# Optimization experiments

Measured on AMD Instinct MI355X. Metric: run time of the kernel, lower is better.

The kernel has to match this reference:

```python
import jax, jax.numpy as jnp
import numpy as np

N_EMBD = 2048
N_HEAD = 32
N_KV_HEADS = 8
HEAD_DIM = 64
N_REP = N_HEAD // N_KV_HEADS
MAX_SEQ_LEN = 4096
ROPE_THETA = 10000.0


def _precompute_freqs_cis(dim, end, theta=ROPE_THETA):
    freqs = 1.0 / theta ** (jnp.arange(0, dim, 2)[: dim // 2].astype(jnp.float32) / dim)
    t = jnp.arange(end, dtype=jnp.float32)
    freqs = jnp.outer(t, freqs)  # (end, dim//2)
    return jnp.cos(freqs), jnp.sin(freqs)


def setup_inputs() -> dict:
    key = jax.random.key(0)
    ks = jax.random.split(key, 5)
    B, S = 2, 2048
    x = jax.random.normal(ks[0], (B, S, N_EMBD), dtype=jnp.float32)
    # torch Linear(in, out, bias=False): y = x @ W.T, W is (out, in). We store (in, out).
    sc = 1.0 / np.sqrt(N_EMBD)
    wq = jax.random.normal(ks[1], (N_EMBD, N_EMBD), dtype=jnp.float32) * sc
    wk = jax.random.normal(ks[2], (N_EMBD, N_KV_HEADS * HEAD_DIM), dtype=jnp.float32) * sc
    wv = jax.random.normal(ks[3], (N_EMBD, N_KV_HEADS * HEAD_DIM), dtype=jnp.float32) * sc
    wo = jax.random.normal(ks[4], (N_EMBD, N_EMBD), dtype=jnp.float32) * sc
    freqs_cos, freqs_sin = _precompute_freqs_cis(HEAD_DIM, MAX_SEQ_LEN)
    return {"x": x, "wq": wq, "wk": wk, "wv": wv, "wo": wo,
            "freqs_cos": freqs_cos, "freqs_sin": freqs_sin}


def _apply_rotary(t, cos, sin):
    # t: (B, S, H, HD); interleaved real/imag pairs along last dim.
    shp = t.shape
    t2 = t.reshape(*shp[:-1], HEAD_DIM // 2, 2)
    r, i = t2[..., 0], t2[..., 1]
    out_r = r * cos - i * sin
    out_i = r * sin + i * cos
    return jnp.stack([out_r, out_i], axis=-1).reshape(shp)


def reference(x, wq, wk, wv, wo, freqs_cos, freqs_sin):
    B, S, _ = x.shape
    xq = (x @ wq).reshape(B, S, N_HEAD, HEAD_DIM)
    xk = (x @ wk).reshape(B, S, N_KV_HEADS, HEAD_DIM)
    xv = (x @ wv).reshape(B, S, N_KV_HEADS, HEAD_DIM)

    cos = freqs_cos[:S][None, :, None, :]  # (1, S, 1, HD/2)
    sin = freqs_sin[:S][None, :, None, :]
    xq = _apply_rotary(xq, cos, sin)
    xk = _apply_rotary(xk, cos, sin)

    # GQA: repeat KV heads (repeat_interleave along head dim)
    keys = jnp.repeat(xk, N_REP, axis=2)    # (B, S, H, HD)
    values = jnp.repeat(xv, N_REP, axis=2)

    scores = jnp.einsum('bqhd,bkhd->bhqk', xq, keys) / np.sqrt(HEAD_DIM)
    causal = jnp.tril(jnp.ones((S, S), dtype=bool))
    scores = jnp.where(causal, scores, -jnp.inf)
    probs = jax.nn.softmax(scores.astype(jnp.float32), axis=-1).astype(xq.dtype)
    out = jnp.einsum('bhqk,bkhd->bqhd', probs, values)  # (B, S, H, HD)
    out = out.reshape(B, S, N_EMBD)
    return out @ wo
```

## Files before the change

kernel.cpp:

```cpp
#include <hip/hip_runtime.h>
#include <hip/hip_fp16.h>
#include <stdint.h>

typedef _Float16 f16x8 __attribute__((ext_vector_type(8)));
typedef _Float16 f16x2 __attribute__((ext_vector_type(2)));
typedef float f32x4 __attribute__((ext_vector_type(4)));

#define B_ 2
#define S_ 2048
#define NE 2048
#define NH 32
#define NKV 8
#define HD 64
#define NTOK (B_ * S_)
#define QKVN 3072

__device__ __forceinline__ void gld_lds16(void* lds, const void* g) {
  __builtin_amdgcn_global_load_lds(
      (const __attribute__((address_space(1))) void*)g,
      (__attribute__((address_space(3))) void*)lds, 16, 0, 0);
}

__global__ void conv_x_kernel(const float* __restrict__ x,
                              _Float16* __restrict__ xo, int n2) {
  int i = blockIdx.x * 256 + threadIdx.x;
  if (i < n2) {
    float2 v = ((const float2*)x)[i];
    f16x2 h;
    h.x = (_Float16)v.x;
    h.y = (_Float16)v.y;
    ((f16x2*)xo)[i] = h;
  }
}

__global__ void tconv_kernel(const float* __restrict__ src,
                             _Float16* __restrict__ dst,
                             int srcN, int rowoff, int ldd) {
  __shared__ float tile[32][33];
  int n0 = blockIdx.x * 32, k0 = blockIdx.y * 32;
  int tx = threadIdx.x, ty = threadIdx.y;
  for (int i = ty; i < 32; i += 8)
    tile[i][tx] = src[(size_t)(k0 + i) * srcN + n0 + tx];
  __syncthreads();
  for (int i = ty; i < 32; i += 8)
    dst[(size_t)(rowoff + n0 + i) * ldd + k0 + tx] = (_Float16)tile[tx][i];
}

template <int OUT_F32>
__global__ __launch_bounds__(256, 2) void gemm_bt(
    const _Float16* __restrict__ A, const _Float16* __restrict__ Bt,
    void* __restrict__ Cout, int M, int N, int K) {
  __shared__ _Float16 As[128 * 32];
  __shared__ _Float16 Bs[128 * 32];
  const int tid = threadIdx.x;
  const int wave = tid >> 6, lane = tid & 63;
  const int qd = lane >> 4, ln = lane & 15;
  const int m0 = blockIdx.y * 128, n0 = blockIdx.x * 128;
  const int wm = (wave >> 1) * 64, wn = (wave & 1) * 64;

  f32x4 acc[4][4] = {};

  const int srow = (lane >> 2);
  const int scol = (lane & 3) * 8;

  for (int k0 = 0; k0 < K; k0 += 32) {
    __syncthreads();
#pragma unroll
    for (int it = 0; it < 2; ++it) {
      int r = wave * 32 + it * 16 + srow;
      gld_lds16(&As[(wave * 32 + it * 16) * 32],
                A + (size_t)(m0 + r) * K + k0 + scol);
      gld_lds16(&Bs[(wave * 32 + it * 16) * 32],
                Bt + (size_t)(n0 + r) * K + k0 + scol);
    }
    __syncthreads();
    f16x8 a[4], b[4];
#pragma unroll
    for (int mt = 0; mt < 4; ++mt)
      a[mt] = *(const f16x8*)&As[(wm + mt * 16 + ln) * 32 + qd * 8];
#pragma unroll
    for (int nt = 0; nt < 4; ++nt)
      b[nt] = *(const f16x8*)&Bs[(wn + nt * 16 + ln) * 32 + qd * 8];
#pragma unroll
    for (int mt = 0; mt < 4; ++mt)
#pragma unroll
      for (int nt = 0; nt < 4; ++nt)
        acc[mt][nt] =
            __builtin_amdgcn_mfma_f32_16x16x32_f16(a[mt], b[nt], acc[mt][nt], 0, 0, 0);
  }

#pragma unroll
  for (int mt = 0; mt < 4; ++mt) {
    int row = m0 + wm + mt * 16 + qd * 4;
#pragma unroll
    for (int nt = 0; nt < 4; ++nt) {
      int col = n0 + wn + nt * 16 + ln;
#pragma unroll
      for (int r = 0; r < 4; ++r) {
        if (OUT_F32)
          ((float*)Cout)[(size_t)(row + r) * N + col] = acc[mt][nt][r];
        else
          ((_Float16*)Cout)[(size_t)(row + r) * N + col] =
              (_Float16)acc[mt][nt][r];
      }
    }
  }
}

__global__ void rope_scatter_kernel(const _Float16* __restrict__ qkv,
                                    const float* __restrict__ fcos,
                                    const float* __restrict__ fsin,
                                    _Float16* __restrict__ Qb,
                                    _Float16* __restrict__ Kb) {
  const float QSC = 0.125f * 1.44269504088896f;
  int idx = blockIdx.x * 256 + threadIdx.x;
  int t = idx / 1280;
  int col = (idx - t * 1280) * 2;
  int b = t >> 11, s = t & 2047;
  float v0 = (float)qkv[(size_t)t * QKVN + col];
  float v1 = (float)qkv[(size_t)t * QKVN + col + 1];
  _Float16* dst;
  size_t off;
  int d;
  float sc;
  if (col < 2048) {
    int h = col >> 6;
    d = col & 63;
    dst = Qb;
    off = ((size_t)(b * NH + h) * S_ + s) * HD + d;
    sc = QSC;
  } else {
    int cc = col - 2048;
    int h = cc >> 6;
    d = cc & 63;
    dst = Kb;
    off = ((size_t)(b * NKV + h) * S_ + s) * HD + d;
    sc = 1.0f;
  }
  float c = fcos[s * 32 + (d >> 1)], sn = fsin[s * 32 + (d >> 1)];
  f16x2 o;
  o.x = (_Float16)((v0 * c - v1 * sn) * sc);
  o.y = (_Float16)((v0 * sn + v1 * c) * sc);
  *(f16x2*)(dst + off) = o;
}

__global__ void vtrans_kernel(const _Float16* __restrict__ qkv,
                              _Float16* __restrict__ Vtg) {
  __shared__ _Float16 tile[64][65];
  int t0 = blockIdx.x * 64;
  int kv = blockIdx.y, b = blockIdx.z;
  int tid = threadIdx.x;
  for (int slot = tid; slot < 4096; slot += 256) {
    int r = slot >> 6, c = slot & 63;
    tile[r][c] = qkv[(size_t)(b * S_ + t0 + r) * QKVN + 2560 + kv * 64 + c];
  }
  __syncthreads();
  size_t base = ((size_t)(b * NKV + kv) * HD) * S_;
  for (int slot = tid; slot < 4096; slot += 256) {
    int d = slot >> 6, r = slot & 63;
    Vtg[base + (size_t)d * S_ + t0 + r] = tile[r][d];
  }
}

__global__ __launch_bounds__(256, 2) void attn_kernel(
    const _Float16* __restrict__ Qb, const _Float16* __restrict__ Kb,
    const _Float16* __restrict__ Vtg, _Float16* __restrict__ Ob) {
  constexpr int LDK = 72;
  constexpr float M_SHIFT = 10.0f;
  __shared__ _Float16 Ks[64 * LDK];
  __shared__ _Float16 Vs[64 * LDK];
  __shared__ _Float16 Ps[4 * 32 * LDK];
  const int tid = threadIdx.x;
  const int wave = tid >> 6, lane = tid & 63;
  const int qd = lane >> 4, ln = lane & 15;
  const int h = blockIdx.y, b = blockIdx.z;
  const int kvh = h >> 2;

  const _Float16* Qh = Qb + ((size_t)(b * NH + h) * S_) * HD;
  const _Float16* Kh = Kb + ((size_t)(b * NKV + kvh) * S_) * HD;
  const _Float16* Vh = Vtg + ((size_t)(b * NKV + kvh) * HD) * S_;

  const int sr = tid >> 3;
  const int sc = (tid & 7) * 8;
  _Float16* Pw = &Ps[wave * 32 * LDK];

#pragma unroll
  for (int pass = 0; pass < 2; ++pass) {
    const int qt = pass ? blockIdx.x : (15 - blockIdx.x);
    const int q0 = qt * 128;
    const int nkt = 2 * qt + 2;

    f16x8 aq[2][2];
#pragma unroll
    for (int mt = 0; mt < 2; ++mt) {
      int qrow = q0 + mt * 64 + wave * 16 + ln;
      aq[mt][0] = *(const f16x8*)(Qh + (size_t)qrow * HD + qd * 8);
      aq[mt][1] = *(const f16x8*)(Qh + (size_t)qrow * HD + 32 + qd * 8);
    }

    f32x4 accO[2][4] = {};
    float lsum[2][4] = {};

    f16x8 kp[2], vp[2];
#pragma unroll
    for (int i = 0; i < 2; ++i) {
      kp[i] = *(const f16x8*)(Kh + (size_t)(i * 32 + sr) * HD + sc);
      vp[i] = *(const f16x8*)(Vh + (size_t)(i * 32 + sr) * S_ + sc);
    }
#pragma unroll
    for (int i = 0; i < 2; ++i) {
      *(f16x8*)&Ks[(i * 32 + sr) * LDK + sc] = kp[i];
      *(f16x8*)&Vs[(i * 32 + sr) * LDK + sc] = vp[i];
    }

    for (int kt = 0; kt < nkt; ++kt) {
      __syncthreads();
      if (kt + 1 < nkt) {
#pragma unroll
        for (int i = 0; i < 2; ++i) {
          kp[i] = *(const f16x8*)(Kh +
                                  (size_t)((kt + 1) * 64 + i * 32 + sr) * HD + sc);
          vp[i] = *(const f16x8*)(Vh + (size_t)(i * 32 + sr) * S_ +
                                  (kt + 1) * 64 + sc);
        }
      }

      f32x4 s[2][4];
#pragma unroll
      for (int mt = 0; mt < 2; ++mt)
#pragma unroll
        for (int nt = 0; nt < 4; ++nt)
          s[mt][nt] = (f32x4){-M_SHIFT, -M_SHIFT, -M_SHIFT, -M_SHIFT};
#pragma unroll
      for (int nt = 0; nt < 4; ++nt) {
        f16x8 b0 = *(const f16x8*)&Ks[(nt * 16 + ln) * LDK + qd * 8];
        f16x8 b1 = *(const f16x8*)&Ks[(nt * 16 + ln) * LDK + 32 + qd * 8];
#pragma unroll
        for (int mt = 0; mt < 2; ++mt) {
          s[mt][nt] = __builtin_amdgcn_mfma_f32_16x16x32_f16(aq[mt][0], b0,
                                                             s[mt][nt], 0, 0, 0);
          s[mt][nt] = __builtin_amdgcn_mfma_f32_16x16x32_f16(aq[mt][1], b1,
                                                             s[mt][nt], 0, 0, 0);
        }
      }

      const bool edge = (kt >= nkt - 2);
#pragma unroll
      for (int mt = 0; mt < 2; ++mt)
#pragma unroll
        for (int nt = 0; nt < 4; ++nt)
#pragma unroll
          for (int r = 0; r < 4; ++r) {
            float p = exp2f(s[mt][nt][r]);
            if (edge) {
              int key = kt * 64 + nt * 16 + ln;
              int qr = q0 + mt * 64 + wave * 16 + qd * 4 + r;
              if (key > qr) p = 0.f;
            }
            lsum[mt][r] += p;
            Pw[(mt * 16 + qd * 4 + r) * LDK + nt * 16 + ln] = (_Float16)p;
          }

      asm volatile("s_waitcnt lgkmcnt(0)" ::: "memory");
      f16x8 ap[2][2];
#pragma unroll
      for (int mt = 0; mt < 2; ++mt) {
        ap[mt][0] = *(const f16x8*)&Pw[(mt * 16 + ln) * LDK + qd * 8];
        ap[mt][1] = *(const f16x8*)&Pw[(mt * 16 + ln) * LDK + 32 + qd * 8];
      }
#pragma unroll
      for (int nt = 0; nt < 4; ++nt) {
        f16x8 bv0 = *(const f16x8*)&Vs[(nt * 16 + ln) * LDK + qd * 8];
        f16x8 bv1 = *(const f16x8*)&Vs[(nt * 16 + ln) * LDK + 32 + qd * 8];
#pragma unroll
        for (int mt = 0; mt < 2; ++mt) {
          accO[mt][nt] = __builtin_amdgcn_mfma_f32_16x16x32_f16(
              ap[mt][0], bv0, accO[mt][nt], 0, 0, 0);
          accO[mt][nt] = __builtin_amdgcn_mfma_f32_16x16x32_f16(
              ap[mt][1], bv1, accO[mt][nt], 0, 0, 0);
        }
      }

      __syncthreads();
      if (kt + 1 < nkt) {
#pragma unroll
        for (int i = 0; i < 2; ++i) {
          *(f16x8*)&Ks[(i * 32 + sr) * LDK + sc] = kp[i];
          *(f16x8*)&Vs[(i * 32 + sr) * LDK + sc] = vp[i];
        }
      }
    }

#pragma unroll
    for (int mt = 0; mt < 2; ++mt)
#pragma unroll
      for (int r = 0; r < 4; ++r) {
        float t = lsum[mt][r];
#pragma unroll
        for (int off = 1; off <= 8; off <<= 1) t += __shfl_xor(t, off);
        float inv = 1.f / t;
        int srow = q0 + mt * 64 + wave * 16 + qd * 4 + r;
        size_t base = ((size_t)(b * S_) + srow) * NE + h * HD;
#pragma unroll
        for (int nt = 0; nt < 4; ++nt)
          Ob[base + nt * 16 + ln] = (_Float16)(accO[mt][nt][r] * inv);
      }
  }
}

extern "C" void kernel_launch(void* const* d_in, const int* in_sizes, int n_in,
                              void* d_out, int out_size, void* d_ws,
                              size_t ws_size, hipStream_t stream) {
  const float* x = (const float*)d_in[0];
  const float* wq = (const float*)d_in[1];
  const float* wk = (const float*)d_in[2];
  const float* wv = (const float*)d_in[3];
  const float* wo = (const float*)d_in[4];
  const float* fcos = (const float*)d_in[5];
  const float* fsin = (const float*)d_in[6];

  char* ws = (char*)d_ws;
  _Float16* xb = (_Float16*)(ws);
  _Float16* wqkv_t = (_Float16*)(ws + 16777216);
  _Float16* wo_t = (_Float16*)(ws + 29360128);
  _Float16* qkv = (_Float16*)(ws + 37748736);
  _Float16* Qb = (_Float16*)(ws + 62914560);
  _Float16* Kb = (_Float16*)(ws + 79691776);
  _Float16* Vb = (_Float16*)(ws + 83886080);
  _Float16* Ob = (_Float16*)(ws + 88080384);

  conv_x_kernel<<<16384, 256, 0, stream>>>(x, xb, (NTOK * NE) / 2);

  dim3 tb(32, 8);
  tconv_kernel<<<dim3(64, 64), tb, 0, stream>>>(wq, wqkv_t, 2048, 0, 2048);
  tconv_kernel<<<dim3(16, 64), tb, 0, stream>>>(wk, wqkv_t, 512, 2048, 2048);
  tconv_kernel<<<dim3(16, 64), tb, 0, stream>>>(wv, wqkv_t, 512, 2560, 2048);
  tconv_kernel<<<dim3(64, 64), tb, 0, stream>>>(wo, wo_t, 2048, 0, 2048);

  gemm_bt<0><<<dim3(QKVN / 128, NTOK / 128), 256, 0, stream>>>(
      xb, wqkv_t, qkv, NTOK, QKVN, NE);

  rope_scatter_kernel<<<(NTOK * 1280) / 256, 256, 0, stream>>>(qkv, fcos, fsin,
                                                               Qb, Kb);
  vtrans_kernel<<<dim3(S_ / 64, NKV, B_), 256, 0, stream>>>(qkv, Vb);

  attn_kernel<<<dim3(8, NH, B_), 256, 0, stream>>>(Qb, Kb, Vb, Ob);

  gemm_bt<1><<<dim3(NE / 128, NTOK / 128), 256, 0, stream>>>(
      Ob, wo_t, d_out, NTOK, NE, NE);
}
```

Baseline: 349.9 us.

## Switch attention MFMAs to 32x32x16 tiles with XOR-swizzled K/V LDS layout

Rewrites the attention inner loops to use 32x32x16 f16 MFMA instructions instead of 16x16x32, so each wave owns 32 query rows and the fragment layout changes accordingly. K and V shared-memory tiles drop their row padding and use an XOR swizzle on 16-byte chunks to avoid bank conflicts. The intent is fewer MFMA issues and LDS reads per tile. In exchange the 16-element accumulators raise register pressure, and the row-sum reduction now needs one more shuffle step.

```diff
diff --git a/kernel.cpp b/kernel.cpp
--- a/kernel.cpp
+++ b/kernel.cpp
@@ -5,6 +5,7 @@
 typedef _Float16 f16x8 __attribute__((ext_vector_type(8)));
 typedef _Float16 f16x2 __attribute__((ext_vector_type(2)));
 typedef float f32x4 __attribute__((ext_vector_type(4)));
+typedef float f32x16 __attribute__((ext_vector_type(16)));
 
 #define B_ 2
 #define S_ 2048
@@ -165,14 +166,14 @@
 __global__ __launch_bounds__(256, 2) void attn_kernel(
     const _Float16* __restrict__ Qb, const _Float16* __restrict__ Kb,
     const _Float16* __restrict__ Vtg, _Float16* __restrict__ Ob) {
-  constexpr int LDK = 72;
+  constexpr int LDP = 72;
   constexpr float M_SHIFT = 10.0f;
-  __shared__ _Float16 Ks[64 * LDK];
-  __shared__ _Float16 Vs[64 * LDK];
-  __shared__ _Float16 Ps[4 * 32 * LDK];
+  __shared__ _Float16 Ks[64 * 64];
+  __shared__ _Float16 Vs[64 * 64];
+  __shared__ _Float16 Ps[4 * 32 * LDP];
   const int tid = threadIdx.x;
   const int wave = tid >> 6, lane = tid & 63;
-  const int qd = lane >> 4, ln = lane & 15;
+  const int mrow = lane & 31, half = lane >> 5;
   const int h = blockIdx.y, b = blockIdx.z;
   const int kvh = h >> 2;
 
@@ -181,8 +182,8 @@
   const _Float16* Vh = Vtg + ((size_t)(b * NKV + kvh) * HD) * S_;
 
   const int sr = tid >> 3;
-  const int sc = (tid & 7) * 8;
-  _Float16* Pw = &Ps[wave * 32 * LDK];
+  const int scc = tid & 7;
+  _Float16* Pw = &Ps[wave * 32 * LDP];
 
 #pragma unroll
   for (int pass = 0; pass < 2; ++pass) {
@@ -190,27 +191,26 @@
     const int q0 = qt * 128;
     const int nkt = 2 * qt + 2;
 
-    f16x8 aq[2][2];
-#pragma unroll
-    for (int mt = 0; mt < 2; ++mt) {
-      int qrow = q0 + mt * 64 + wave * 16 + ln;
-      aq[mt][0] = *(const f16x8*)(Qh + (size_t)qrow * HD + qd * 8);
-      aq[mt][1] = *(const f16x8*)(Qh + (size_t)qrow * HD + 32 + qd * 8);
-    }
-
-    f32x4 accO[2][4] = {};
-    float lsum[2][4] = {};
+    const int qrow = q0 + wave * 32 + mrow;
+    f16x8 aq[4];
+#pragma unroll
+    for (int kk = 0; kk < 4; ++kk)
+      aq[kk] = *(const f16x8*)(Qh + (size_t)qrow * HD + kk * 16 + half * 8);
+
+    f32x16 accO[2] = {};
+    float lsum[16] = {};
 
     f16x8 kp[2], vp[2];
 #pragma unroll
     for (int i = 0; i < 2; ++i) {
-      kp[i] = *(const f16x8*)(Kh + (size_t)(i * 32 + sr) * HD + sc);
-      vp[i] = *(const f16x8*)(Vh + (size_t)(i * 32 + sr) * S_ + sc);
+      kp[i] = *(const f16x8*)(Kh + (size_t)(i * 32 + sr) * HD + scc * 8);
+      vp[i] = *(const f16x8*)(Vh + (size_t)(i * 32 + sr) * S_ + scc * 8);
     }
 #pragma unroll
     for (int i = 0; i < 2; ++i) {
-      *(f16x8*)&Ks[(i * 32 + sr) * LDK + sc] = kp[i];
-      *(f16x8*)&Vs[(i * 32 + sr) * LDK + sc] = vp[i];
+      int r = i * 32 + sr;
+      *(f16x8*)&Ks[r * 64 + ((scc ^ (r & 7)) * 8)] = kp[i];
+      *(f16x8*)&Vs[r * 64 + ((scc ^ (r & 7)) * 8)] = vp[i];
     }
 
     for (int kt = 0; kt < nkt; ++kt) {
@@ -219,65 +219,61 @@
 #pragma unroll
         for (int i = 0; i < 2; ++i) {
           kp[i] = *(const f16x8*)(Kh +
-                                  (size_t)((kt + 1) * 64 + i * 32 + sr) * HD + sc);
+                                  (size_t)((kt + 1) * 64 + i * 32 + sr) * HD +
+                                  scc * 8);
           vp[i] = *(const f16x8*)(Vh + (size_t)(i * 32 + sr) * S_ +
-                                  (kt + 1) * 64 + sc);
-        }
-      }
-
-      f32x4 s[2][4];
-#pragma unroll
-      for (int mt = 0; mt < 2; ++mt)
-#pragma unroll
-        for (int nt = 0; nt < 4; ++nt)
-          s[mt][nt] = (f32x4){-M_SHIFT, -M_SHIFT, -M_SHIFT, -M_SHIFT};
-#pragma unroll
-      for (int nt = 0; nt < 4; ++nt) {
-        f16x8 b0 = *(const f16x8*)&Ks[(nt * 16 + ln) * LDK + qd * 8];
-        f16x8 b1 = *(const f16x8*)&Ks[(nt * 16 + ln) * LDK + 32 + qd * 8];
-#pragma unroll
-        for (int mt = 0; mt < 2; ++mt) {
-          s[mt][nt] = __builtin_amdgcn_mfma_f32_16x16x32_f16(aq[mt][0], b0,
-                                                             s[mt][nt], 0, 0, 0);
-          s[mt][nt] = __builtin_amdgcn_mfma_f32_16x16x32_f16(aq[mt][1], b1,
-                                                             s[mt][nt], 0, 0, 0);
+                                  (kt + 1) * 64 + scc * 8);
+        }
+      }
+
+      f32x16 s[2];
+#pragma unroll
+      for (int nt = 0; nt < 2; ++nt)
+#pragma unroll
+        for (int r = 0; r < 16; ++r) s[nt][r] = -M_SHIFT;
+#pragma unroll
+      for (int kk = 0; kk < 4; ++kk) {
+        int c = kk * 2 + half;
+#pragma unroll
+        for (int nt = 0; nt < 2; ++nt) {
+          int key = nt * 32 + mrow;
+          f16x8 bk = *(const f16x8*)&Ks[key * 64 + ((c ^ (key & 7)) * 8)];
+          s[nt] = __builtin_amdgcn_mfma_f32_32x32x16_f16(aq[kk], bk, s[nt],
+                                                         0, 0, 0);
         }
       }
 
       const bool edge = (kt >= nkt - 2);
 #pragma unroll
-      for (int mt = 0; mt < 2; ++mt)
-#pragma unroll
-        for (int nt = 0; nt < 4; ++nt)
-#pragma unroll
-          for (int r = 0; r < 4; ++r) {
-            float p = exp2f(s[mt][nt][r]);
-            if (edge) {
-              int key = kt * 64 + nt * 16 + ln;
-              int qr = q0 + mt * 64 + wave * 16 + qd * 4 + r;
-              if (key > qr) p = 0.f;
-            }
-            lsum[mt][r] += p;
-            Pw[(mt * 16 + qd * 4 + r) * LDK + nt * 16 + ln] = (_Float16)p;
+      for (int nt = 0; nt < 2; ++nt)
+#pragma unroll
+        for (int r = 0; r < 16; ++r) {
+          int rr = (r & 3) + 8 * (r >> 2) + 4 * half;
+          float p = exp2f(s[nt][r]);
+          if (edge) {
+            int key = kt * 64 + nt * 32 + mrow;
+            int qr = q0 + wave * 32 + rr;
+            if (key > qr) p = 0.f;
           }
+          lsum[r] += p;
+          Pw[rr * LDP + nt * 32 + mrow] = (_Float16)p;
+        }
 
       asm volatile("s_waitcnt lgkmcnt(0)" ::: "memory");
-      f16x8 ap[2][2];
-#pragma unroll
-      for (int mt = 0; mt < 2; ++mt) {
-        ap[mt][0] = *(const f16x8*)&Pw[(mt * 16 + ln) * LDK + qd * 8];
-        ap[mt][1] = *(const f16x8*)&Pw[(mt * 16 + ln) * LDK + 32 + qd * 8];
-      }
-#pragma unroll
-      for (int nt = 0; nt < 4; ++nt) {
-        f16x8 bv0 = *(const f16x8*)&Vs[(nt * 16 + ln) * LDK + qd * 8];
-        f16x8 bv1 = *(const f16x8*)&Vs[(nt * 16 + ln) * LDK + 32 + qd * 8];
-#pragma unroll
-        for (int mt = 0; mt < 2; ++mt) {
-          accO[mt][nt] = __builtin_amdgcn_mfma_f32_16x16x32_f16(
-              ap[mt][0], bv0, accO[mt][nt], 0, 0, 0);
-          accO[mt][nt] = __builtin_amdgcn_mfma_f32_16x16x32_f16(
-              ap[mt][1], bv1, accO[mt][nt], 0, 0, 0);
+      f16x8 ap[4];
+#pragma unroll
+      for (int kk = 0; kk < 4; ++kk)
+        ap[kk] = *(const f16x8*)&Pw[mrow * LDP + kk * 16 + half * 8];
+
+#pragma unroll
+      for (int kk = 0; kk < 4; ++kk) {
+        int c = kk * 2 + half;
+#pragma unroll
+        for (int nt = 0; nt < 2; ++nt) {
+          int d = nt * 32 + mrow;
+          f16x8 bv = *(const f16x8*)&Vs[d * 64 + ((c ^ (d & 7)) * 8)];
+          accO[nt] = __builtin_amdgcn_mfma_f32_32x32x16_f16(ap[kk], bv,
+                                                            accO[nt], 0, 0, 0);
         }
       }
 
@@ -285,26 +281,26 @@
       if (kt + 1 < nkt) {
 #pragma unroll
         for (int i = 0; i < 2; ++i) {
-          *(f16x8*)&Ks[(i * 32 + sr) * LDK + sc] = kp[i];
-          *(f16x8*)&Vs[(i * 32 + sr) * LDK + sc] = vp[i];
-        }
-      }
-    }
-
-#pragma unroll
-    for (int mt = 0; mt < 2; ++mt)
-#pragma unroll
-      for (int r = 0; r < 4; ++r) {
-        float t = lsum[mt][r];
-#pragma unroll
-        for (int off = 1; off <= 8; off <<= 1) t += __shfl_xor(t, off);
-        float inv = 1.f / t;
-        int srow = q0 + mt * 64 + wave * 16 + qd * 4 + r;
-        size_t base = ((size_t)(b * S_) + srow) * NE + h * HD;
-#pragma unroll
-        for (int nt = 0; nt < 4; ++nt)
-          Ob[base + nt * 16 + ln] = (_Float16)(accO[mt][nt][r] * inv);
-      }
+          int r = i * 32 + sr;
+          *(f16x8*)&Ks[r * 64 + ((scc ^ (r & 7)) * 8)] = kp[i];
+          *(f16x8*)&Vs[r * 64 + ((scc ^ (r & 7)) * 8)] = vp[i];
+        }
+      }
+    }
+
+#pragma unroll
+    for (int r = 0; r < 16; ++r) {
+      float t = lsum[r];
+#pragma unroll
+      for (int off = 1; off <= 16; off <<= 1) t += __shfl_xor(t, off);
+      float inv = 1.f / t;
+      int rr = (r & 3) + 8 * (r >> 2) + 4 * half;
+      int srow = q0 + wave * 32 + rr;
+      size_t base = ((size_t)(b * S_) + srow) * NE + h * HD;
+#pragma unroll
+      for (int nt = 0; nt < 2; ++nt)
+        Ob[base + nt * 32 + mrow] = (_Float16)(accO[nt][r] * inv);
+    }
   }
 }
 
```

Result: no change. 346.2 us (-1.1%).
